# Kernel tuning notes

Hardware: AMD Instinct MI355X
Metric: run time of the kernel (lower is better)

## Reference

```python
import jax, jax.numpy as jnp
import numpy as np

N_NODES = 100000
N_EDGES = 1600000
N_EMBED = 48
N_CONVS = 6
N_GRAPHS = 1000
VOCAB = 100


def setup_inputs() -> dict:
    key = jax.random.key(0)
    ks = jax.random.split(key, 20)
    AtomicNum = jax.random.randint(ks[0], (N_NODES,), 0, VOCAB)
    Edge = jax.random.randint(ks[1], (2, N_EDGES), 0, N_NODES)
    graph_id = jnp.sort(jax.random.randint(ks[2], (N_NODES,), 0, N_GRAPHS))
    s = 1.0 / np.sqrt(N_EMBED)
    def lin(k):
        k1, k2 = jax.random.split(k)
        w = jax.random.uniform(k1, (N_EMBED, N_EMBED), jnp.float32, -s, s)
        b = jax.random.uniform(k2, (N_EMBED,), jnp.float32, -s, s)
        return w, b
    def stacked(k):
        ws, bs = zip(*[lin(kk) for kk in jax.random.split(k, N_CONVS)])
        return jnp.stack(ws), jnp.stack(bs)
    emb = jax.random.normal(ks[3], (VOCAB, N_EMBED), jnp.float32)
    msg_w1, msg_b1 = stacked(ks[4])
    msg_w2, msg_b2 = stacked(ks[5])
    upd_w1, upd_b1 = stacked(ks[6])
    upd_w2, upd_b2 = stacked(ks[7])
    ro_w1, ro_b1 = lin(ks[8])
    k1, k2 = jax.random.split(ks[9])
    ro_w2 = jax.random.uniform(k1, (N_EMBED, 1), jnp.float32, -s, s)
    ro_b2 = jax.random.uniform(k2, (1,), jnp.float32, -s, s)
    return dict(AtomicNum=AtomicNum, Edge=Edge, graph_id=graph_id, emb=emb,
                msg_w1=msg_w1, msg_b1=msg_b1, msg_w2=msg_w2, msg_b2=msg_b2,
                upd_w1=upd_w1, upd_b1=upd_b1, upd_w2=upd_w2, upd_b2=upd_b2,
                ro_w1=ro_w1, ro_b1=ro_b1, ro_w2=ro_w2, ro_b2=ro_b2)


def reference(AtomicNum, Edge, graph_id, emb,
              msg_w1, msg_b1, msg_w2, msg_b2,
              upd_w1, upd_b1, upd_w2, upd_b2,
              ro_w1, ro_b1, ro_w2, ro_b2):
    n_nodes = AtomicNum.shape[0]
    src, dst = Edge[0], Edge[1]
    h = emb[AtomicNum]  # [N, d]
    for l in range(N_CONVS):
        # gather endpoint features, elementwise product, message MLP
        x = h[src] * h[dst]                                      # [E, d]
        m = jax.nn.relu(x @ msg_w1[l] + msg_b1[l]) @ msg_w2[l] + msg_b2[l]
        agg = jax.ops.segment_sum(m, dst, num_segments=n_nodes)  # scatter_add
        u = jax.nn.relu(agg @ upd_w1[l] + upd_b1[l]) @ upd_w2[l] + upd_b2[l]
        h = h + u  # residual update
    y = jax.nn.relu(h @ ro_w1 + ro_b1) @ ro_w2 + ro_b2           # [N, 1]
    # per-graph sum readout (== torch.split by Natom + sum per chunk)
    out = jax.ops.segment_sum(y[:, 0], graph_id, num_segments=N_GRAPHS)
    return out
```

## Files before the change

### kernel.cpp

```cpp
#include <hip/hip_runtime.h>
#include <hip/hip_bf16.h>


#define NE 48
#define NB_SH 8

typedef __attribute__((ext_vector_type(8))) short short8;
typedef __attribute__((ext_vector_type(4))) float floatx4;

__device__ __forceinline__ unsigned short bf16_rne(float v) {
    unsigned u = __float_as_uint(v);
    u += 0x7FFFu + ((u >> 16) & 1u);
    return (unsigned short)(u >> 16);
}

__device__ __forceinline__ void split8p(const float* __restrict__ x, short8& hi, short8& lo) {
    union { unsigned u[4]; short8 s; } H, L;
#pragma unroll
    for (int i = 0; i < 4; ++i) {
        float a = x[2 * i], b = x[2 * i + 1];
        __hip_bfloat162 h2 = __float22bfloat162_rn(make_float2(a, b));
        unsigned h = *reinterpret_cast<unsigned*>(&h2);
        float ra = a - __uint_as_float(h << 16);
        float rb = b - __uint_as_float(h & 0xFFFF0000u);
        __hip_bfloat162 l2 = __float22bfloat162_rn(make_float2(ra, rb));
        H.u[i] = h;
        L.u[i] = *reinterpret_cast<unsigned*>(&l2);
    }
    hi = H.s; lo = L.s;
}

__device__ __forceinline__ void gemm3(const short8& ah0, const short8& al0,
                                      const short8& ah1, const short8& al1,
                                      const short8* __restrict__ hi,
                                      const short8* __restrict__ lo,
                                      int lane, floatx4* acc) {
#pragma unroll
    for (int t = 0; t < 3; ++t) {
        short8 bh0 = hi[(t * 2 + 0) * 64 + lane];
        short8 bh1 = hi[(t * 2 + 1) * 64 + lane];
        short8 bl0 = lo[(t * 2 + 0) * 64 + lane];
        short8 bl1 = lo[(t * 2 + 1) * 64 + lane];
        floatx4 c = {0.0f, 0.0f, 0.0f, 0.0f};
        c = __builtin_amdgcn_mfma_f32_16x16x32_bf16(ah0, bh0, c, 0, 0, 0);
        c = __builtin_amdgcn_mfma_f32_16x16x32_bf16(ah1, bh1, c, 0, 0, 0);
        c = __builtin_amdgcn_mfma_f32_16x16x32_bf16(al0, bh0, c, 0, 0, 0);
        c = __builtin_amdgcn_mfma_f32_16x16x32_bf16(al1, bh1, c, 0, 0, 0);
        c = __builtin_amdgcn_mfma_f32_16x16x32_bf16(ah0, bl0, c, 0, 0, 0);
        c = __builtin_amdgcn_mfma_f32_16x16x32_bf16(ah1, bl1, c, 0, 0, 0);
        acc[t] = c;
    }
}

__global__ __launch_bounds__(256) void embed_kernel(const int* __restrict__ an,
                                                    const float* __restrict__ emb,
                                                    float* __restrict__ h, int n4) {
    int i = blockIdx.x * 256 + threadIdx.x;
    if (i >= n4) return;
    int n = i / 12, q = i - n * 12;
    ((float4*)h)[i] = ((const float4*)emb)[an[n] * 12 + q];
}

__global__ __launch_bounds__(256) void hist_kernel(const int* __restrict__ dst,
                                                   int* __restrict__ cnt, int E) {
    int e = blockIdx.x * 256 + threadIdx.x;
    if (e < E) atomicAdd(&cnt[dst[e]], 1);
}

__global__ __launch_bounds__(256) void scansum_kernel(const int* __restrict__ cnt,
                                                      int* __restrict__ bsum, int N) {
    __shared__ int sw[4];
    const int tid = threadIdx.x, lane = tid & 63, wid = tid >> 6;
    int base = blockIdx.x * 1024;
    int v = 0;
#pragma unroll
    for (int k = 0; k < 4; ++k) {
        int i = base + k * 256 + tid;
        v += (i < N) ? cnt[i] : 0;
    }
#pragma unroll
    for (int o = 1; o < 64; o <<= 1) v += __shfl_xor(v, o, 64);
    if (lane == 0) sw[wid] = v;
    __syncthreads();
    if (tid == 0) bsum[blockIdx.x] = sw[0] + sw[1] + sw[2] + sw[3];
}

__global__ __launch_bounds__(256) void scanb_kernel(int* __restrict__ bsum, int nblk) {
    __shared__ int s[256];
    int tid = threadIdx.x;
    s[tid] = (tid < nblk) ? bsum[tid] : 0;
    __syncthreads();
    if (tid == 0) {
        int run = 0;
        for (int i = 0; i < nblk; ++i) { int t = s[i]; s[i] = run; run += t; }
    }
    __syncthreads();
    if (tid < nblk) bsum[tid] = s[tid];
}

__global__ __launch_bounds__(1024) void scanfix_kernel(const int* __restrict__ cnt,
                                                       const int* __restrict__ bsum,
                                                       int* __restrict__ offs,
                                                       int* __restrict__ gpos, int N) {
    __shared__ int swave[16];
    const int tid = threadIdx.x, lane = tid & 63, wid = tid >> 6;
    int i = blockIdx.x * 1024 + tid;
    int orig = (i < N) ? cnt[i] : 0;
    int v = orig;
#pragma unroll
    for (int off = 1; off < 64; off <<= 1) {
        int u = __shfl_up(v, off, 64);
        if (lane >= off) v += u;
    }
    if (lane == 63) swave[wid] = v;
    __syncthreads();
    if (wid == 0) {
        int w = (lane < 16) ? swave[lane] : 0;
#pragma unroll
        for (int off = 1; off < 16; off <<= 1) {
            int u = __shfl_up(w, off, 64);
            if (lane >= off) w += u;
        }
        if (lane < 16) swave[lane] = w;
    }
    __syncthreads();
    int prefix = (wid > 0) ? swave[wid - 1] : 0;
    int val = bsum[blockIdx.x] + prefix + v - orig;
    if (i < N) {
        offs[i] = val;
        if ((i & 255) == 0) gpos[i >> 8] = val;
    }
}

__global__ __launch_bounds__(256) void partA_kernel(const int* __restrict__ src,
                                                    const int* __restrict__ dst,
                                                    int* __restrict__ gpos,
                                                    int2* __restrict__ pairbuf,
                                                    int E, int NB) {
    __shared__ int lhist[512];
    __shared__ int lbase[512];
    const int tid = threadIdx.x;
    for (int i = tid; i < NB; i += 256) lhist[i] = 0;
    __syncthreads();
    const int base = blockIdx.x * 2048;
    int ssrc[8], sdst[8], rnk[8];
#pragma unroll
    for (int k = 0; k < 8; ++k) {
        int e = base + k * 256 + tid;
        if (e < E) {
            ssrc[k] = src[e]; sdst[k] = dst[e];
            rnk[k] = atomicAdd(&lhist[sdst[k] >> NB_SH], 1);
        }
    }
    __syncthreads();
    for (int i = tid; i < NB; i += 256) {
        int c = lhist[i];
        lbase[i] = c ? atomicAdd(&gpos[i], c) : 0;
    }
    __syncthreads();
#pragma unroll
    for (int k = 0; k < 8; ++k) {
        int e = base + k * 256 + tid;
        if (e < E)
            pairbuf[lbase[sdst[k] >> NB_SH] + rnk[k]] = make_int2(ssrc[k], sdst[k]);
    }
}

__global__ __launch_bounds__(256) void partB_kernel(const int2* __restrict__ pairbuf,
                                                    int* __restrict__ offs,
                                                    int* __restrict__ colsrc, int E) {
    int e = blockIdx.x * 256 + threadIdx.x;
    if (e < E) {
        int2 p = pairbuf[e];
        int pos = atomicAdd(&offs[p.y], 1);
        colsrc[pos] = p.x;
    }
}

__global__ __launch_bounds__(256) void pack_all_kernel(const float* __restrict__ w0,
                                                       const float* __restrict__ w1m,
                                                       const float* __restrict__ w2m,
                                                       const float* __restrict__ w3m,
                                                       const float* __restrict__ w4m,
                                                       short8* __restrict__ hi,
                                                       short8* __restrict__ lo) {
    int idx = blockIdx.x * 256 + threadIdx.x;
    if (idx >= 4 * 2304 + 384) return;
    int slot = idx / 2304;
    int rem  = idx - slot * 2304;
    const float* w = (slot == 0) ? w0 : (slot == 1) ? w1m : (slot == 2) ? w2m
                   : (slot == 3) ? w3m : w4m;
    int lane = rem & 63;
    int s = (rem >> 6) & 1;
    int t = (rem >> 7) % 3;
    int l = (rem >> 7) / 3;
    short8 h8, l8;
#pragma unroll
    for (int i = 0; i < 8; ++i) {
        int k = s * 32 + (lane >> 4) * 8 + i;
        int j = t * 16 + (lane & 15);
        float v = (k < NE) ? w[l * NE * NE + k * NE + j] : 0.0f;
        unsigned short hh = bf16_rne(v);
        float hf = __uint_as_float((unsigned)hh << 16);
        unsigned short ll = bf16_rne(v - hf);
        h8[i] = (short)hh;
        l8[i] = (short)ll;
    }
    hi[idx] = h8;
    lo[idx] = l8;
}

__global__ __launch_bounds__(64, 4) void edge_kernel(
    const float* __restrict__ hin,
    const int* __restrict__ colsrc,
    const int* __restrict__ ends,
    const int* __restrict__ cnt,
    float* __restrict__ tagg,
    const short8* __restrict__ bhi,
    const short8* __restrict__ blo,
    const float* __restrict__ b1,
    int N)
{
    const int lane = threadIdx.x;
    const int n0 = blockIdx.x * 4;
    if (n0 >= N) return;

    const int m  = lane & 15;
    const int kb = lane >> 4;

    short8 bh[6], bl[6];
#pragma unroll
    for (int i = 0; i < 6; ++i) { bh[i] = bhi[i * 64 + lane]; bl[i] = blo[i * 64 + lane]; }
    const float bb0 = b1[m], bb1 = b1[16 + m], bb2 = b1[32 + m];

#pragma unroll 1
    for (int nn = 0; nn < 4; ++nn) {
        const int n = n0 + nn;
        const int deg = cnt[n];
        const int end = ends[n];
        const int beg = end - deg;

        const float* hd = hin + (size_t)n * NE;
        float4 d0a = ((const float4*)(hd + kb * 8))[0];
        float4 d0b = ((const float4*)(hd + kb * 8))[1];
        float4 d1a = make_float4(0, 0, 0, 0), d1b = d1a;
        if (kb < 2) {
            d1a = ((const float4*)(hd + 32 + kb * 8))[0];
            d1b = ((const float4*)(hd + 32 + kb * 8))[1];
        }

        float s0 = 0.0f, s1 = 0.0f, s2 = 0.0f;
        const int ntile = (deg + 15) >> 4;

        for (int it = 0; it < ntile; ++it) {
            const int rem = deg - it * 16;
            int eidx = beg + it * 16 + m;
            int srow = colsrc[(m < rem) ? eidx : beg];
            const float* hs = hin + (size_t)srow * NE + kb * 8;

            float x0[8], x1[8];
            {
                float4 a0 = ((const float4*)hs)[0];
                float4 a1 = ((const float4*)hs)[1];
                x0[0] = a0.x * d0a.x; x0[1] = a0.y * d0a.y; x0[2] = a0.z * d0a.z; x0[3] = a0.w * d0a.w;
                x0[4] = a1.x * d0b.x; x0[5] = a1.y * d0b.y; x0[6] = a1.z * d0b.z; x0[7] = a1.w * d0b.w;
            }
            if (kb < 2) {
                float4 a0 = ((const float4*)(hs + 32))[0];
                float4 a1 = ((const float4*)(hs + 32))[1];
                x1[0] = a0.x * d1a.x; x1[1] = a0.y * d1a.y; x1[2] = a0.z * d1a.z; x1[3] = a0.w * d1a.w;
                x1[4] = a1.x * d1b.x; x1[5] = a1.y * d1b.y; x1[6] = a1.z * d1b.z; x1[7] = a1.w * d1b.w;
            } else {
#pragma unroll
                for (int i = 0; i < 8; ++i) x1[i] = 0.0f;
            }

            short8 ah0, al0, ah1, al1;
            split8p(x0, ah0, al0);
            split8p(x1, ah1, al1);

#pragma unroll
            for (int t = 0; t < 3; ++t) {
                short8 bh0 = bh[t * 2 + 0], bh1 = bh[t * 2 + 1];
                short8 bl0 = bl[t * 2 + 0], bl1 = bl[t * 2 + 1];
                floatx4 c = {0.0f, 0.0f, 0.0f, 0.0f};
                c = __builtin_amdgcn_mfma_f32_16x16x32_bf16(ah0, bh0, c, 0, 0, 0);
                c = __builtin_amdgcn_mfma_f32_16x16x32_bf16(ah1, bh1, c, 0, 0, 0);
                c = __builtin_amdgcn_mfma_f32_16x16x32_bf16(al0, bh0, c, 0, 0, 0);
                c = __builtin_amdgcn_mfma_f32_16x16x32_bf16(al1, bh1, c, 0, 0, 0);
                c = __builtin_amdgcn_mfma_f32_16x16x32_bf16(ah0, bl0, c, 0, 0, 0);
                c = __builtin_amdgcn_mfma_f32_16x16x32_bf16(ah1, bl1, c, 0, 0, 0);
                const float bb = (t == 0) ? bb0 : (t == 1) ? bb1 : bb2;
                float ts = 0.0f;
#pragma unroll
                for (int r = 0; r < 4; ++r) {
                    float v = fmaxf(c[r] + bb, 0.0f);
                    v = (kb * 4 + r < rem) ? v : 0.0f;
                    ts += v;
                }
                if (t == 0) s0 += ts; else if (t == 1) s1 += ts; else s2 += ts;
            }
        }

        s0 += __shfl_xor(s0, 16, 64); s0 += __shfl_xor(s0, 32, 64);
        s1 += __shfl_xor(s1, 16, 64); s1 += __shfl_xor(s1, 32, 64);
        s2 += __shfl_xor(s2, 16, 64); s2 += __shfl_xor(s2, 32, 64);

        float t1 = __shfl(s1, lane & 15, 64);
        float t2 = __shfl(s2, lane & 15, 64);
        float val = (lane < 16) ? s0 : (lane < 32) ? t1 : t2;
        if (lane < 48) tagg[(size_t)n * NE + lane] = val;
    }
}

__global__ __launch_bounds__(64, 4) void node_kernel(
    const float* __restrict__ hin,
    float* __restrict__ hout,
    const int* __restrict__ cnt,
    const short8* __restrict__ w2hi, const short8* __restrict__ w2lo, const float* __restrict__ b2,
    const short8* __restrict__ u1hi, const short8* __restrict__ u1lo, const float* __restrict__ ub1,
    const short8* __restrict__ u2hi, const short8* __restrict__ u2lo, const float* __restrict__ ub2,
    int N,
    int final_layer,
    const int* __restrict__ gid,
    const short8* __restrict__ rw1hi, const short8* __restrict__ rw1lo,
    const float* __restrict__ rb1, const float* __restrict__ rw2,
    const float* __restrict__ rb2, float* __restrict__ out)
{
    __shared__ float tile[16][52];
    const int lane = threadIdx.x;
    const int n0 = blockIdx.x * 16;
    if (n0 >= N) return;

    const int m  = lane & 15;
    const int kb = lane >> 4;

    float c0[8], c1[8];
    {
        const float* tg = hout + (size_t)(n0 + m) * NE;
        *(float4*)(c0)     = *(const float4*)(tg + kb * 8);
        *(float4*)(c0 + 4) = *(const float4*)(tg + kb * 8 + 4);
        if (kb < 2) {
            *(float4*)(c1)     = *(const float4*)(tg + 32 + kb * 8);
            *(float4*)(c1 + 4) = *(const float4*)(tg + 32 + kb * 8 + 4);
        } else {
#pragma unroll
            for (int i = 0; i < 8; ++i) c1[i] = 0.0f;
        }
    }
    short8 ah0, al0, ah1, al1;
    split8p(c0, ah0, al0);
    split8p(c1, ah1, al1);

    floatx4 acc[3];
    gemm3(ah0, al0, ah1, al1, w2hi, w2lo, lane, acc);

    {
        float b2j[3];
#pragma unroll
        for (int t = 0; t < 3; ++t) b2j[t] = b2[t * 16 + m];
#pragma unroll
        for (int r = 0; r < 4; ++r) {
            float fd = (float)cnt[n0 + kb * 4 + r];
#pragma unroll
            for (int t = 0; t < 3; ++t) acc[t][r] = fmaf(fd, b2j[t], acc[t][r]);
        }
    }

#pragma unroll
    for (int t = 0; t < 3; ++t)
#pragma unroll
        for (int r = 0; r < 4; ++r)
            tile[kb * 4 + r][t * 16 + m] = acc[t][r];
    asm volatile("s_waitcnt lgkmcnt(0)" ::: "memory");
    {
        const float* row = &tile[m][0];
        *(float4*)(c0)     = *(const float4*)(row + kb * 8);
        *(float4*)(c0 + 4) = *(const float4*)(row + kb * 8 + 4);
        if (kb < 2) {
            *(float4*)(c1)     = *(const float4*)(row + 32 + kb * 8);
            *(float4*)(c1 + 4) = *(const float4*)(row + 32 + kb * 8 + 4);
        } else {
#pragma unroll
            for (int i = 0; i < 8; ++i) c1[i] = 0.0f;
        }
    }
    asm volatile("s_waitcnt lgkmcnt(0)" ::: "memory");
    split8p(c0, ah0, al0);
    split8p(c1, ah1, al1);
    gemm3(ah0, al0, ah1, al1, u1hi, u1lo, lane, acc);
    {
        float bj[3];
#pragma unroll
        for (int t = 0; t < 3; ++t) bj[t] = ub1[t * 16 + m];
#pragma unroll
        for (int t = 0; t < 3; ++t)
#pragma unroll
            for (int r = 0; r < 4; ++r)
                acc[t][r] = fmaxf(acc[t][r] + bj[t], 0.0f);
    }

#pragma unroll
    for (int t = 0; t < 3; ++t)
#pragma unroll
        for (int r = 0; r < 4; ++r)
            tile[kb * 4 + r][t * 16 + m] = acc[t][r];
    asm volatile("s_waitcnt lgkmcnt(0)" ::: "memory");
    {
        const float* row = &tile[m][0];
        *(float4*)(c0)     = *(const float4*)(row + kb * 8);
        *(float4*)(c0 + 4) = *(const float4*)(row + kb * 8 + 4);
        if (kb < 2) {
            *(float4*)(c1)     = *(const float4*)(row + 32 + kb * 8);
            *(float4*)(c1 + 4) = *(const float4*)(row + 32 + kb * 8 + 4);
        } else {
#pragma unroll
            for (int i = 0; i < 8; ++i) c1[i] = 0.0f;
        }
    }
    asm volatile("s_waitcnt lgkmcnt(0)" ::: "memory");
    split8p(c0, ah0, al0);
    split8p(c1, ah1, al1);
    gemm3(ah0, al0, ah1, al1, u2hi, u2lo, lane, acc);

    {
        float bj[3];
#pragma unroll
        for (int t = 0; t < 3; ++t) bj[t] = ub2[t * 16 + m];
#pragma unroll
        for (int r = 0; r < 4; ++r) {
            const size_t row = (size_t)(n0 + kb * 4 + r) * NE;
#pragma unroll
            for (int t = 0; t < 3; ++t)
                acc[t][r] += hin[row + t * 16 + m] + bj[t];
        }
    }

    if (!final_layer) {
#pragma unroll
        for (int r = 0; r < 4; ++r) {
            const size_t row = (size_t)(n0 + kb * 4 + r) * NE;
#pragma unroll
            for (int t = 0; t < 3; ++t)
                hout[row + t * 16 + m] = acc[t][r];
        }
        return;
    }

#pragma unroll
    for (int t = 0; t < 3; ++t)
#pragma unroll
        for (int r = 0; r < 4; ++r)
            tile[kb * 4 + r][t * 16 + m] = acc[t][r];
    asm volatile("s_waitcnt lgkmcnt(0)" ::: "memory");
    {
        const float* row = &tile[m][0];
        *(float4*)(c0)     = *(const float4*)(row + kb * 8);
        *(float4*)(c0 + 4) = *(const float4*)(row + kb * 8 + 4);
        if (kb < 2) {
            *(float4*)(c1)     = *(const float4*)(row + 32 + kb * 8);
            *(float4*)(c1 + 4) = *(const float4*)(row + 32 + kb * 8 + 4);
        } else {
#pragma unroll
            for (int i = 0; i < 8; ++i) c1[i] = 0.0f;
        }
    }
    split8p(c0, ah0, al0);
    split8p(c1, ah1, al1);
    gemm3(ah0, al0, ah1, al1, rw1hi, rw1lo, lane, acc);

    float p[4] = {0.0f, 0.0f, 0.0f, 0.0f};
    {
        float bj[3], wj[3];
#pragma unroll
        for (int t = 0; t < 3; ++t) { bj[t] = rb1[t * 16 + m]; wj[t] = rw2[t * 16 + m]; }
#pragma unroll
        for (int t = 0; t < 3; ++t)
#pragma unroll
            for (int r = 0; r < 4; ++r)
                p[r] = fmaf(fmaxf(acc[t][r] + bj[t], 0.0f), wj[t], p[r]);
    }
#pragma unroll
    for (int o = 1; o < 16; o <<= 1) {
#pragma unroll
        for (int r = 0; r < 4; ++r) p[r] += __shfl_xor(p[r], o, 16);
    }
    if (m == 0) {
        float b2v = rb2[0];
#pragma unroll
        for (int r = 0; r < 4; ++r) {
            int n = n0 + kb * 4 + r;
            atomicAdd(out + gid[n], p[r] + b2v);
        }
    }
}

extern "C" void kernel_launch(void* const* d_in, const int* in_sizes, int n_in,
                              void* d_out, int out_size, void* d_ws, size_t ws_size,
                              hipStream_t stream) {
    const int*   AtomicNum = (const int*)  d_in[0];
    const int*   Edge      = (const int*)  d_in[1];
    const int*   graph_id  = (const int*)  d_in[2];
    const float* emb       = (const float*)d_in[3];
    const float* msg_w1    = (const float*)d_in[4];
    const float* msg_b1    = (const float*)d_in[5];
    const float* msg_w2    = (const float*)d_in[6];
    const float* msg_b2    = (const float*)d_in[7];
    const float* upd_w1    = (const float*)d_in[8];
    const float* upd_b1    = (const float*)d_in[9];
    const float* upd_w2    = (const float*)d_in[10];
    const float* upd_b2    = (const float*)d_in[11];
    const float* ro_w1     = (const float*)d_in[12];
    const float* ro_b1     = (const float*)d_in[13];
    const float* ro_w2     = (const float*)d_in[14];
    const float* ro_b2     = (const float*)d_in[15];

    const int N = in_sizes[0];
    const int E = in_sizes[1] / 2;
    const int* src = Edge;
    const int* dst = Edge + E;
    const int NB = (N + 255) >> NB_SH;
    const int NBLK = (N + 1023) / 1024;

    float*  h    = (float*)d_ws;
    float*  h2   = h  + (size_t)N * NE;
    int*    cnt  = (int*)(h2 + (size_t)N * NE);
    int*    offs = cnt + N;
    int*    colsrc = offs + N;
    short8* whi  = (short8*)(colsrc + E);
    short8* wlo  = whi + (4 * 2304 + 384);
    int*    gpos = (int*)(wlo + (4 * 2304 + 384));
    int*    bsum = gpos + NB;
    int2*   pairbuf = (int2*)h2;

    hipMemsetAsync(d_out, 0, (size_t)out_size * sizeof(float), stream);
    hipMemsetAsync(cnt, 0, (size_t)N * sizeof(int), stream);

    int n4 = N * 12;
    embed_kernel<<<(n4 + 255) / 256, 256, 0, stream>>>(AtomicNum, emb, h, n4);

    hist_kernel<<<(E + 255) / 256, 256, 0, stream>>>(dst, cnt, E);
    scansum_kernel<<<NBLK, 256, 0, stream>>>(cnt, bsum, N);
    scanb_kernel<<<1, 256, 0, stream>>>(bsum, NBLK);
    scanfix_kernel<<<NBLK, 1024, 0, stream>>>(cnt, bsum, offs, gpos, N);
    partA_kernel<<<(E + 2047) / 2048, 256, 0, stream>>>(src, dst, gpos, pairbuf, E, NB);
    partB_kernel<<<(E + 255) / 256, 256, 0, stream>>>(pairbuf, offs, colsrc, E);

    pack_all_kernel<<<(4 * 2304 + 384 + 255) / 256, 256, 0, stream>>>(
        msg_w1, msg_w2, upd_w1, upd_w2, ro_w1, whi, wlo);

    const float* hin = h;
    float* hout = h2;
    for (int l = 0; l < 6; ++l) {
        edge_kernel<<<N / 4, 64, 0, stream>>>(
            hin, colsrc, offs, cnt, hout,
            whi + 0 * 2304 + (size_t)l * 384, wlo + 0 * 2304 + (size_t)l * 384,
            msg_b1 + (size_t)l * NE,
            N);
        node_kernel<<<N / 16, 64, 0, stream>>>(
            hin, hout, cnt,
            whi + 1 * 2304 + (size_t)l * 384, wlo + 1 * 2304 + (size_t)l * 384, msg_b2 + (size_t)l * NE,
            whi + 2 * 2304 + (size_t)l * 384, wlo + 2 * 2304 + (size_t)l * 384, upd_b1 + (size_t)l * NE,
            whi + 3 * 2304 + (size_t)l * 384, wlo + 3 * 2304 + (size_t)l * 384, upd_b2 + (size_t)l * NE,
            N,
            (l == 5) ? 1 : 0,
            graph_id,
            whi + 4 * 2304, wlo + 4 * 2304,
            ro_b1, ro_w2, ro_b2, (float*)d_out);
        const float* tmp = hin; hin = hout; hout = (float*)tmp;
    }
}
```

Baseline: 823.4 us.

## Fuse edge and node kernels into one per-layer kernel via LDS tile

Merges the per-layer edge aggregation kernel and the node MLP kernel into one kernel. Each wave aggregates 16 nodes and writes the hidden sums into its own LDS tile instead of global memory, then runs the node GEMMs straight from that tile. This removes a global write and read of the aggregated tensor and one launch per layer. In exchange the block size grows to 256, each wave does 16 nodes of edge work with more variable per-wave load, and occupancy changes under the new launch bounds.

```diff
diff --git a/kernel.cpp b/kernel.cpp
--- a/kernel.cpp
+++ b/kernel.cpp
@@ -210,23 +210,35 @@
     lo[idx] = l8;
 }
 
-__global__ __launch_bounds__(64, 4) void edge_kernel(
+__global__ __launch_bounds__(256, 2) void layer_kernel(
     const float* __restrict__ hin,
     const int* __restrict__ colsrc,
     const int* __restrict__ ends,
     const int* __restrict__ cnt,
-    float* __restrict__ tagg,
+    float* __restrict__ hout,
     const short8* __restrict__ bhi,
     const short8* __restrict__ blo,
     const float* __restrict__ b1,
-    int N)
+    const short8* __restrict__ w2hi, const short8* __restrict__ w2lo, const float* __restrict__ b2,
+    const short8* __restrict__ u1hi, const short8* __restrict__ u1lo, const float* __restrict__ ub1,
+    const short8* __restrict__ u2hi, const short8* __restrict__ u2lo, const float* __restrict__ ub2,
+    int N,
+    int final_layer,
+    const int* __restrict__ gid,
+    const short8* __restrict__ rw1hi, const short8* __restrict__ rw1lo,
+    const float* __restrict__ rb1, const float* __restrict__ rw2,
+    const float* __restrict__ rb2, float* __restrict__ out)
 {
-    const int lane = threadIdx.x;
-    const int n0 = blockIdx.x * 4;
+    __shared__ float tile[4][16][52];
+    const int tid  = threadIdx.x;
+    const int lane = tid & 63;
+    const int wid  = tid >> 6;
+    const int n0   = blockIdx.x * 64 + wid * 16;
     if (n0 >= N) return;
 
     const int m  = lane & 15;
     const int kb = lane >> 4;
+    float (*mytile)[52] = tile[wid];
 
     short8 bh[6], bl[6];
 #pragma unroll
@@ -234,7 +246,7 @@
     const float bb0 = b1[m], bb1 = b1[16 + m], bb2 = b1[32 + m];
 
 #pragma unroll 1
-    for (int nn = 0; nn < 4; ++nn) {
+    for (int nn = 0; nn < 16; ++nn) {
         const int n = n0 + nn;
         const int deg = cnt[n];
         const int end = ends[n];
@@ -306,75 +318,16 @@
         s1 += __shfl_xor(s1, 16, 64); s1 += __shfl_xor(s1, 32, 64);
         s2 += __shfl_xor(s2, 16, 64); s2 += __shfl_xor(s2, 32, 64);
 
-        float t1 = __shfl(s1, lane & 15, 64);
-        float t2 = __shfl(s2, lane & 15, 64);
-        float val = (lane < 16) ? s0 : (lane < 32) ? t1 : t2;
-        if (lane < 48) tagg[(size_t)n * NE + lane] = val;
-    }
-}
-
-__global__ __launch_bounds__(64, 4) void node_kernel(
-    const float* __restrict__ hin,
-    float* __restrict__ hout,
-    const int* __restrict__ cnt,
-    const short8* __restrict__ w2hi, const short8* __restrict__ w2lo, const float* __restrict__ b2,
-    const short8* __restrict__ u1hi, const short8* __restrict__ u1lo, const float* __restrict__ ub1,
-    const short8* __restrict__ u2hi, const short8* __restrict__ u2lo, const float* __restrict__ ub2,
-    int N,
-    int final_layer,
-    const int* __restrict__ gid,
-    const short8* __restrict__ rw1hi, const short8* __restrict__ rw1lo,
-    const float* __restrict__ rb1, const float* __restrict__ rw2,
-    const float* __restrict__ rb2, float* __restrict__ out)
-{
-    __shared__ float tile[16][52];
-    const int lane = threadIdx.x;
-    const int n0 = blockIdx.x * 16;
-    if (n0 >= N) return;
-
-    const int m  = lane & 15;
-    const int kb = lane >> 4;
+        float t1v = __shfl(s1, lane & 15, 64);
+        float t2v = __shfl(s2, lane & 15, 64);
+        float val = (lane < 16) ? s0 : (lane < 32) ? t1v : t2v;
+        if (lane < 48) mytile[nn][lane] = val;
+    }
+    asm volatile("s_waitcnt lgkmcnt(0)" ::: "memory");
 
     float c0[8], c1[8];
     {
-        const float* tg = hout + (size_t)(n0 + m) * NE;
-        *(float4*)(c0)     = *(const float4*)(tg + kb * 8);
-        *(float4*)(c0 + 4) = *(const float4*)(tg + kb * 8 + 4);
-        if (kb < 2) {
-            *(float4*)(c1)     = *(const float4*)(tg + 32 + kb * 8);
-            *(float4*)(c1 + 4) = *(const float4*)(tg + 32 + kb * 8 + 4);
-        } else {
-#pragma unroll
-            for (int i = 0; i < 8; ++i) c1[i] = 0.0f;
-        }
-    }
-    short8 ah0, al0, ah1, al1;
-    split8p(c0, ah0, al0);
-    split8p(c1, ah1, al1);
-
-    floatx4 acc[3];
-    gemm3(ah0, al0, ah1, al1, w2hi, w2lo, lane, acc);
-
-    {
-        float b2j[3];
-#pragma unroll
-        for (int t = 0; t < 3; ++t) b2j[t] = b2[t * 16 + m];
-#pragma unroll
-        for (int r = 0; r < 4; ++r) {
-            float fd = (float)cnt[n0 + kb * 4 + r];
-#pragma unroll
-            for (int t = 0; t < 3; ++t) acc[t][r] = fmaf(fd, b2j[t], acc[t][r]);
-        }
-    }
-
-#pragma unroll
-    for (int t = 0; t < 3; ++t)
-#pragma unroll
-        for (int r = 0; r < 4; ++r)
-            tile[kb * 4 + r][t * 16 + m] = acc[t][r];
-    asm volatile("s_waitcnt lgkmcnt(0)" ::: "memory");
-    {
-        const float* row = &tile[m][0];
+        const float* row = &mytile[m][0];
         *(float4*)(c0)     = *(const float4*)(row + kb * 8);
         *(float4*)(c0 + 4) = *(const float4*)(row + kb * 8 + 4);
         if (kb < 2) {
@@ -386,28 +339,33 @@
         }
     }
     asm volatile("s_waitcnt lgkmcnt(0)" ::: "memory");
+    short8 ah0, al0, ah1, al1;
     split8p(c0, ah0, al0);
     split8p(c1, ah1, al1);
-    gemm3(ah0, al0, ah1, al1, u1hi, u1lo, lane, acc);
-    {
-        float bj[3];
-#pragma unroll
-        for (int t = 0; t < 3; ++t) bj[t] = ub1[t * 16 + m];
-#pragma unroll
-        for (int t = 0; t < 3; ++t)
-#pragma unroll
-            for (int r = 0; r < 4; ++r)
-                acc[t][r] = fmaxf(acc[t][r] + bj[t], 0.0f);
+
+    floatx4 acc[3];
+    gemm3(ah0, al0, ah1, al1, w2hi, w2lo, lane, acc);
+
+    {
+        float b2j[3];
+#pragma unroll
+        for (int t = 0; t < 3; ++t) b2j[t] = b2[t * 16 + m];
+#pragma unroll
+        for (int r = 0; r < 4; ++r) {
+            float fd = (float)cnt[n0 + kb * 4 + r];
+#pragma unroll
+            for (int t = 0; t < 3; ++t) acc[t][r] = fmaf(fd, b2j[t], acc[t][r]);
+        }
     }
 
 #pragma unroll
     for (int t = 0; t < 3; ++t)
 #pragma unroll
         for (int r = 0; r < 4; ++r)
-            tile[kb * 4 + r][t * 16 + m] = acc[t][r];
-    asm volatile("s_waitcnt lgkmcnt(0)" ::: "memory");
-    {
-        const float* row = &tile[m][0];
+            mytile[kb * 4 + r][t * 16 + m] = acc[t][r];
+    asm volatile("s_waitcnt lgkmcnt(0)" ::: "memory");
+    {
+        const float* row = &mytile[m][0];
         *(float4*)(c0)     = *(const float4*)(row + kb * 8);
         *(float4*)(c0 + 4) = *(const float4*)(row + kb * 8 + 4);
         if (kb < 2) {
@@ -421,6 +379,39 @@
     asm volatile("s_waitcnt lgkmcnt(0)" ::: "memory");
     split8p(c0, ah0, al0);
     split8p(c1, ah1, al1);
+    gemm3(ah0, al0, ah1, al1, u1hi, u1lo, lane, acc);
+    {
+        float bj[3];
+#pragma unroll
+        for (int t = 0; t < 3; ++t) bj[t] = ub1[t * 16 + m];
+#pragma unroll
+        for (int t = 0; t < 3; ++t)
+#pragma unroll
+            for (int r = 0; r < 4; ++r)
+                acc[t][r] = fmaxf(acc[t][r] + bj[t], 0.0f);
+    }
+
+#pragma unroll
+    for (int t = 0; t < 3; ++t)
+#pragma unroll
+        for (int r = 0; r < 4; ++r)
+            mytile[kb * 4 + r][t * 16 + m] = acc[t][r];
+    asm volatile("s_waitcnt lgkmcnt(0)" ::: "memory");
+    {
+        const float* row = &mytile[m][0];
+        *(float4*)(c0)     = *(const float4*)(row + kb * 8);
+        *(float4*)(c0 + 4) = *(const float4*)(row + kb * 8 + 4);
+        if (kb < 2) {
+            *(float4*)(c1)     = *(const float4*)(row + 32 + kb * 8);
+            *(float4*)(c1 + 4) = *(const float4*)(row + 32 + kb * 8 + 4);
+        } else {
+#pragma unroll
+            for (int i = 0; i < 8; ++i) c1[i] = 0.0f;
+        }
+    }
+    asm volatile("s_waitcnt lgkmcnt(0)" ::: "memory");
+    split8p(c0, ah0, al0);
+    split8p(c1, ah1, al1);
     gemm3(ah0, al0, ah1, al1, u2hi, u2lo, lane, acc);
 
     {
@@ -451,10 +442,10 @@
     for (int t = 0; t < 3; ++t)
 #pragma unroll
         for (int r = 0; r < 4; ++r)
-            tile[kb * 4 + r][t * 16 + m] = acc[t][r];
-    asm volatile("s_waitcnt lgkmcnt(0)" ::: "memory");
-    {
-        const float* row = &tile[m][0];
+            mytile[kb * 4 + r][t * 16 + m] = acc[t][r];
+    asm volatile("s_waitcnt lgkmcnt(0)" ::: "memory");
+    {
+        const float* row = &mytile[m][0];
         *(float4*)(c0)     = *(const float4*)(row + kb * 8);
         *(float4*)(c0 + 4) = *(const float4*)(row + kb * 8 + 4);
         if (kb < 2) {
@@ -552,13 +543,10 @@
     const float* hin = h;
     float* hout = h2;
     for (int l = 0; l < 6; ++l) {
-        edge_kernel<<<N / 4, 64, 0, stream>>>(
+        layer_kernel<<<(N + 63) / 64, 256, 0, stream>>>(
             hin, colsrc, offs, cnt, hout,
             whi + 0 * 2304 + (size_t)l * 384, wlo + 0 * 2304 + (size_t)l * 384,
             msg_b1 + (size_t)l * NE,
-            N);
-        node_kernel<<<N / 16, 64, 0, stream>>>(
-            hin, hout, cnt,
             whi + 1 * 2304 + (size_t)l * 384, wlo + 1 * 2304 + (size_t)l * 384, msg_b2 + (size_t)l * NE,
             whi + 2 * 2304 + (size_t)l * 384, wlo + 2 * 2304 + (size_t)l * 384, upd_b1 + (size_t)l * NE,
             whi + 3 * 2304 + (size_t)l * 384, wlo + 3 * 2304 + (size_t)l * 384, upd_b2 + (size_t)l * NE,
```

Measured after the change: 870.0 us. 1.06x slower.
